# Kernel tuning notes

Measured on AMD Instinct MI355X. Metric: run time of the kernel, lower is better.

## Reference

```python
import jax, jax.numpy as jnp
import numpy as np

B, INDIM, OUTDIM = 4096, 640, 64
EPS = 1e-6


def setup_inputs() -> dict:
    key = jax.random.key(0)
    k1, k2 = jax.random.split(key)
    x = jax.random.normal(k1, (B, INDIM), dtype=jnp.float32)
    # weight_v of nn.Linear(indim, outdim): shape [outdim, indim]
    weight_v = jax.random.normal(k2, (OUTDIM, INDIM), dtype=jnp.float32) / np.sqrt(INDIM)
    # temp initialized to zeros(1) - 1
    temp = jnp.full((1,), -1.0, dtype=jnp.float32)
    return {"x": x, "weight_v": weight_v, "temp": temp}


def reference(x, weight_v, temp):
    # x: [B, indim]; weight_v: [outdim, indim]; temp: [1]
    # L2-normalize rows of (x + eps), exactly as torch.norm(x + 1e-6, dim=1)
    xn = x / jnp.linalg.norm(x + EPS, axis=1, keepdims=True)  # [B, indim]
    outdim, indim = weight_v.shape
    # Faithful to torch: transpose THEN row-major reshape (scrambles layout
    # unless indim == outdim).
    w = weight_v.T.reshape(1, outdim, indim)  # [1, outdim, indim]
    diff = xn[:, None, :] - w                 # [B, outdim, indim] (large intermediate)
    dist = jnp.sqrt(jnp.sum(diff * diff, axis=2))  # [B, outdim]
    return temp * dist
```

## Files before the change

kernel.cpp:

```cpp
#include <hip/hip_runtime.h>
#include <math.h>

typedef short bf16x8 __attribute__((ext_vector_type(8)));
typedef float f32x4 __attribute__((ext_vector_type(4)));

static __device__ __forceinline__ unsigned cvt_pk_bf16(float lo, float hi) {
    unsigned r;
    asm("v_cvt_pk_bf16_f32 %0, %1, %2" : "=v"(r) : "v"(lo), "v"(hi));
    return r;
}

__global__ __launch_bounds__(1024) void fused_all(
    const float* __restrict__ x, const float* __restrict__ wv,
    const float* __restrict__ temp, float* __restrict__ out) {
    __shared__ __align__(16) short wf[40960];
    __shared__ f32x4 ldsacc[3][4][64];
    __shared__ float ldsn[4][16];
    __shared__ float ldsnw[4][4][16];

    const int tid = threadIdx.x;
    const int l = tid & 63, lm = l & 15, lg = l >> 4;
    const int w = tid >> 6;
    const int ct = w & 3, kseg = w >> 2;
    const int rt = blockIdx.x;

    const int cg = (tid & 7) | (((tid >> 5) & 7) << 3);
    const int rp0 = ((tid >> 3) & 3) | (((tid >> 8) & 3) << 2);
    float2 va[2][5], vb[2][5];
#pragma unroll
    for (int it = 0; it < 2; ++it) {
        const int rp = rp0 | (it << 4);
        const float* r0 = wv + (2 * rp) * 640 + 10 * cg;
        const float* r1 = r0 + 640;
#pragma unroll
        for (int j = 0; j < 5; ++j) {
            va[it][j] = *(const float2*)(r0 + 2 * j);
            vb[it][j] = *(const float2*)(r1 + 2 * j);
        }
    }

    const float* xr = x + (rt * 16 + lm) * 640 + kseg * 160 + lg * 8;
    float4 xa[10];
#pragma unroll
    for (int s = 0; s < 5; ++s) {
        xa[2 * s]     = *(const float4*)(xr + s * 32);
        xa[2 * s + 1] = *(const float4*)(xr + s * 32 + 4);
    }
    float tv = temp[0];

#pragma unroll
    for (int it = 0; it < 2; ++it) {
        const int rp = rp0 | (it << 4);
        char* base = (char*)wf + (rp >> 4) * 4096 + (cg >> 4) * 1024 +
                     (cg & 15) * 16 + ((rp >> 2) & 3) * 256 + 4 * (rp & 3);
#pragma unroll
        for (int j = 0; j < 5; ++j) {
            *(unsigned*)(base + (2 * j) * 8192) =
                cvt_pk_bf16(va[it][j].x, vb[it][j].x);
            *(unsigned*)(base + (2 * j + 1) * 8192) =
                cvt_pk_bf16(va[it][j].y, vb[it][j].y);
        }
    }
    __syncthreads();

    const bf16x8* wfq = (const bf16x8*)wf;
    const int qb = (kseg * 20 + ct) * 64 + l;

    f32x4 acc  = {0.f, 0.f, 0.f, 0.f};
    f32x4 accW = {0.f, 0.f, 0.f, 0.f};
    f32x4 accG = {0.f, 0.f, 0.f, 0.f};
#pragma unroll
    for (int s = 0; s < 5; ++s) {
        bf16x8 b = wfq[qb + s * 256];
        float4 a0 = xa[2 * s], a1 = xa[2 * s + 1];
        union { unsigned u[4]; bf16x8 v; } A;
        A.u[0] = cvt_pk_bf16(a0.x, a0.y);
        A.u[1] = cvt_pk_bf16(a0.z, a0.w);
        A.u[2] = cvt_pk_bf16(a1.x, a1.y);
        A.u[3] = cvt_pk_bf16(a1.z, a1.w);
        acc  = __builtin_amdgcn_mfma_f32_16x16x32_bf16(A.v, b, acc, 0, 0, 0);
        accW = __builtin_amdgcn_mfma_f32_16x16x32_bf16(b, b, accW, 0, 0, 0);
        if (ct == 0)
            accG = __builtin_amdgcn_mfma_f32_16x16x32_bf16(A.v, A.v, accG, 0, 0, 0);
    }

    if ((lm >> 2) == lg) {
        ldsnw[kseg][ct][lm] = accW[lm & 3];
        if (ct == 0) ldsn[kseg][lm] = accG[lm & 3];
    }
    if (kseg > 0) ldsacc[kseg - 1][ct][l] = acc;
    __syncthreads();

    if (kseg == 0) {
#pragma unroll
        for (int p = 0; p < 3; ++p) {
            f32x4 t2 = ldsacc[p][ct][l];
            acc[0] += t2[0]; acc[1] += t2[1]; acc[2] += t2[2]; acc[3] += t2[3];
        }
        float nwv = ldsnw[0][ct][lm] + ldsnw[1][ct][lm] +
                    ldsnw[2][ct][lm] + ldsnw[3][ct][lm];
#pragma unroll
        for (int i = 0; i < 4; ++i) {
            int rr = lg * 4 + i;
            float S2 = ldsn[0][rr] + ldsn[1][rr] + ldsn[2][rr] + ldsn[3][rr];
            float iv = rsqrtf(S2);
            float d2 = 1.0f - 2.f * acc[i] * iv + nwv;
            out[(rt * 16 + rr) * 64 + ct * 16 + lm] = tv * sqrtf(fmaxf(d2, 0.f));
        }
    }
}

extern "C" void kernel_launch(void* const* d_in, const int* in_sizes, int n_in,
                              void* d_out, int out_size, void* d_ws, size_t ws_size,
                              hipStream_t stream) {
    const float* x = (const float*)d_in[0];
    const float* wv = (const float*)d_in[1];
    const float* temp = (const float*)d_in[2];
    float* out = (float*)d_out;

    fused_all<<<256, 1024, 0, stream>>>(x, wv, temp, out);
}
```

Baseline: 13.71 us.

## Split column tiles across blocks: 1024 blocks of 256 threads

Instead of one 1024-thread block computing all four 16-column tiles for a 16-row tile, each 256-thread block now handles a single column tile. The grid grows to 1024 blocks, each staging only its quarter of the bf16 weight matrix in LDS. This spreads work over more CUs and shrinks per-block LDS and sync scope. In exchange, each x row tile is loaded four times and the x-norm MFMA is recomputed in every block.

```diff
diff --git a/kernel.cpp b/kernel.cpp
--- a/kernel.cpp
+++ b/kernel.cpp
@@ -10,27 +10,27 @@
     return r;
 }
 
-__global__ __launch_bounds__(1024) void fused_all(
+__global__ __launch_bounds__(256, 4) void fused_all(
     const float* __restrict__ x, const float* __restrict__ wv,
     const float* __restrict__ temp, float* __restrict__ out) {
-    __shared__ __align__(16) short wf[40960];
-    __shared__ f32x4 ldsacc[3][4][64];
+    __shared__ __align__(16) short wf[10240];
+    __shared__ f32x4 ldsacc[3][64];
     __shared__ float ldsn[4][16];
-    __shared__ float ldsnw[4][4][16];
+    __shared__ float ldsnw[4][16];
 
     const int tid = threadIdx.x;
     const int l = tid & 63, lm = l & 15, lg = l >> 4;
-    const int w = tid >> 6;
-    const int ct = w & 3, kseg = w >> 2;
-    const int rt = blockIdx.x;
+    const int kseg = tid >> 6;
+    const int bid = blockIdx.x;
+    const int rt = bid & 255, ct = bid >> 8;
 
-    const int cg = (tid & 7) | (((tid >> 5) & 7) << 3);
-    const int rp0 = ((tid >> 3) & 3) | (((tid >> 8) & 3) << 2);
+    const int cg = tid & 15;
+    const int rp0 = (tid >> 4) & 15;
     float2 va[2][5], vb[2][5];
 #pragma unroll
     for (int it = 0; it < 2; ++it) {
         const int rp = rp0 | (it << 4);
-        const float* r0 = wv + (2 * rp) * 640 + 10 * cg;
+        const float* r0 = wv + (2 * rp) * 640 + (16 * ct + cg) * 10;
         const float* r1 = r0 + 640;
 #pragma unroll
         for (int j = 0; j < 5; ++j) {
@@ -51,27 +51,27 @@
 #pragma unroll
     for (int it = 0; it < 2; ++it) {
         const int rp = rp0 | (it << 4);
-        char* base = (char*)wf + (rp >> 4) * 4096 + (cg >> 4) * 1024 +
-                     (cg & 15) * 16 + ((rp >> 2) & 3) * 256 + 4 * (rp & 3);
+        char* base = (char*)wf + (rp >> 4) * 1024 + ((rp >> 2) & 3) * 256 +
+                     cg * 16 + 4 * (rp & 3);
 #pragma unroll
         for (int j = 0; j < 5; ++j) {
-            *(unsigned*)(base + (2 * j) * 8192) =
+            *(unsigned*)(base + (2 * j) * 2048) =
                 cvt_pk_bf16(va[it][j].x, vb[it][j].x);
-            *(unsigned*)(base + (2 * j + 1) * 8192) =
+            *(unsigned*)(base + (2 * j + 1) * 2048) =
                 cvt_pk_bf16(va[it][j].y, vb[it][j].y);
         }
     }
     __syncthreads();
 
     const bf16x8* wfq = (const bf16x8*)wf;
-    const int qb = (kseg * 20 + ct) * 64 + l;
+    const int qb = kseg * 5 * 64 + l;
 
     f32x4 acc  = {0.f, 0.f, 0.f, 0.f};
     f32x4 accW = {0.f, 0.f, 0.f, 0.f};
     f32x4 accG = {0.f, 0.f, 0.f, 0.f};
 #pragma unroll
     for (int s = 0; s < 5; ++s) {
-        bf16x8 b = wfq[qb + s * 256];
+        bf16x8 b = wfq[qb + s * 64];
         float4 a0 = xa[2 * s], a1 = xa[2 * s + 1];
         union { unsigned u[4]; bf16x8 v; } A;
         A.u[0] = cvt_pk_bf16(a0.x, a0.y);
@@ -80,25 +80,23 @@
         A.u[3] = cvt_pk_bf16(a1.z, a1.w);
         acc  = __builtin_amdgcn_mfma_f32_16x16x32_bf16(A.v, b, acc, 0, 0, 0);
         accW = __builtin_amdgcn_mfma_f32_16x16x32_bf16(b, b, accW, 0, 0, 0);
-        if (ct == 0)
-            accG = __builtin_amdgcn_mfma_f32_16x16x32_bf16(A.v, A.v, accG, 0, 0, 0);
+        accG = __builtin_amdgcn_mfma_f32_16x16x32_bf16(A.v, A.v, accG, 0, 0, 0);
     }
 
     if ((lm >> 2) == lg) {
-        ldsnw[kseg][ct][lm] = accW[lm & 3];
-        if (ct == 0) ldsn[kseg][lm] = accG[lm & 3];
+        ldsnw[kseg][lm] = accW[lm & 3];
+        ldsn[kseg][lm]  = accG[lm & 3];
     }
-    if (kseg > 0) ldsacc[kseg - 1][ct][l] = acc;
+    if (kseg > 0) ldsacc[kseg - 1][l] = acc;
     __syncthreads();
 
     if (kseg == 0) {
 #pragma unroll
         for (int p = 0; p < 3; ++p) {
-            f32x4 t2 = ldsacc[p][ct][l];
+            f32x4 t2 = ldsacc[p][l];
             acc[0] += t2[0]; acc[1] += t2[1]; acc[2] += t2[2]; acc[3] += t2[3];
         }
-        float nwv = ldsnw[0][ct][lm] + ldsnw[1][ct][lm] +
-                    ldsnw[2][ct][lm] + ldsnw[3][ct][lm];
+        float nwv = ldsnw[0][lm] + ldsnw[1][lm] + ldsnw[2][lm] + ldsnw[3][lm];
 #pragma unroll
         for (int i = 0; i < 4; ++i) {
             int rr = lg * 4 + i;
@@ -118,5 +116,5 @@
     const float* temp = (const float*)d_in[2];
     float* out = (float*)d_out;
 
-    fused_all<<<256, 1024, 0, stream>>>(x, wv, temp, out);
+    fused_all<<<1024, 256, 0, stream>>>(x, wv, temp, out);
 }
```

Result: no change. 13.56 us (-1.1%).
